# Performance work log

Hardware: AMD Instinct MI355X
Metric: run time of the kernel (lower is better)

The kernel has to match this reference:

```python
import jax, jax.numpy as jnp
import numpy as np

NEG = -1e30  # log-domain 'zero' (safe stand-in for -inf)


def _ctc_loss(logits, labels, label_length, logit_length):
    """Dense-label CTC loss, blank = last class, logits [B,T,C] batch-major.

    Matches tf.nn.ctc_loss(blank_index=-1, logits_time_major=False):
    per-example negative log-likelihood via the standard forward algorithm
    on the blank-extended label sequence of length S = 2L+1.
    """
    B, T, C = logits.shape
    L = labels.shape[1]
    S = 2 * L + 1
    blank = C - 1

    logp = jax.nn.log_softmax(logits, axis=-1)           # [B,T,C]
    lp_t = jnp.moveaxis(logp, 1, 0)                      # [T,B,C]

    # Extended label: blank, l1, blank, l2, ..., blank
    y_ext = jnp.full((B, S), blank, dtype=labels.dtype).at[:, 1::2].set(labels)
    s_idx = jnp.arange(S)
    # s -> s-2 skip allowed iff current symbol is a non-blank differing from s-2
    y_m2 = jnp.pad(y_ext, ((0, 0), (2, 0)), constant_values=blank)[:, :-2]
    skip = (s_idx[None, :] >= 2) & (y_ext != blank) & (y_ext != y_m2)  # [B,S]

    emit0 = jnp.take_along_axis(lp_t[0], y_ext, axis=1)  # [B,S]
    alpha0 = jnp.where(s_idx[None, :] <= 1, emit0, NEG)  # paths start at s=0 or 1

    def step(alpha, lp):
        emit = jnp.take_along_axis(lp, y_ext, axis=1)                      # [B,S]
        a1 = jnp.pad(alpha, ((0, 0), (1, 0)), constant_values=NEG)[:, :-1]  # s-1
        a2 = jnp.pad(alpha, ((0, 0), (2, 0)), constant_values=NEG)[:, :-2]  # s-2
        a2 = jnp.where(skip, a2, NEG)
        new = jnp.logaddexp(jnp.logaddexp(alpha, a1), a2) + emit
        return new, new

    _, alphas = jax.lax.scan(step, alpha0, lp_t[1:])     # [T-1,B,S]
    alphas = jnp.concatenate([alpha0[None], alphas], axis=0)  # [T,B,S]

    b = jnp.arange(B)
    final = alphas[logit_length - 1, b]                  # [B,S] alpha at last frame
    end = 2 * label_length                               # index of final blank
    nll = -jnp.logaddexp(final[b, end], final[b, end - 1])
    return jnp.mean(nll)


def setup_inputs() -> dict:
    key = jax.random.key(0)
    k1, k2, k3 = jax.random.split(key, 3)
    B, T, C, L = 256, 256, 512, 64
    logits = jax.random.normal(k1, (B, T, C), dtype=jnp.float32)
    labels = jax.random.randint(k2, (B, L), 0, C - 1, dtype=jnp.int32)  # never blank
    label_length = jax.random.randint(k3, (B,), 16, L + 1, dtype=jnp.int32)
    logit_length = jnp.full((B,), T, dtype=jnp.int32)
    return {"logits": logits, "labels": labels,
            "label_length": label_length, "logit_length": logit_length}


def reference(logits, labels, label_length, logit_length):
    return _ctc_loss(logits, labels, label_length, logit_length)
```

## Files before the change

kernel.cpp:

```cpp
#include <hip/hip_runtime.h>
#include <math.h>

#define NEGV -1e30f

constexpr int Bc = 256;
constexpr int Tc = 256;
constexpr int Cc = 512;
constexpr int Lc = 64;
constexpr int GR = 8;
constexpr int NGRP = Tc / GR;
constexpr float INVLN2 = 1.44269504088896340736f;
constexpr float LN2    = 0.69314718055994530942f;

__device__ __forceinline__ float la2(float a, float b) {
    float m = fmaxf(a, b);
    float d = fabsf(a - b);
    return m + __log2f(exp2f(-d) + 1.0f);
}

__device__ __forceinline__ float dpp_shr1(float x, float fill) {
    int r = __builtin_amdgcn_update_dpp(__float_as_int(fill), __float_as_int(x),
                                        0x138 , 0xF, 0xF, false);
    return __int_as_float(r);
}

__global__ __launch_bounds__(256) void ctc_k(const float* __restrict__ logits,
                                             const int* __restrict__ labels,
                                             const int* __restrict__ lab_len,
                                             const int* __restrict__ log_len,
                                             float* __restrict__ nll) {
    const int b    = blockIdx.x;
    const int tid  = threadIdx.x;
    const int w    = tid >> 6;
    const int lane = tid & 63;

    __shared__ float rows[2][GR][Cc];
    __shared__ float em_l[2][GR][64];
    __shared__ float em_b[2][GR];

    const float* base = logits + (size_t)b * Tc * Cc;
    const int y = labels[b * Lc + lane];

    const int  prevlab = __shfl_up(y, 1, 64);
    const bool skip    = (lane >= 1) && (y != prevlab);
    const int  llm1    = log_len[b] - 1;
    float ae = NEGV, ao = NEGV, ax = NEGV;
    float fe = NEGV, fo = NEGV, fx = NEGV;

    auto step = [&](float em_lv, float em_bv, int t) {
        float q  = la2(ao, ae);
        float x2 = la2(ax, ao);
        float po = dpp_shr1(ao, NEGV);
        float nae = la2(ae, po) + em_bv;
        float nao = (skip ? la2(q, po) : q) + em_lv;
        float nax = x2 + em_bv;
        ae = nae; ao = nao; ax = nax;
        if (t == llm1) { fe = ae; fo = ao; fx = ax; }
    };

    float4 A0, A1, A2, A3;
    float4 B0, B1, B2, B3;

    auto issue = [&](int g, float4& r0a, float4& r0b, float4& r1a, float4& r1b) {
        const float4* p0 = (const float4*)(base + (size_t)(g * GR + w) * Cc);
        const float4* p1 = (const float4*)(base + (size_t)(g * GR + w + 4) * Cc);
        r0a = p0[lane]; r0b = p0[lane + 64];
        r1a = p1[lane]; r1b = p1[lane + 64];
    };

    auto row_em = [&](int s, int r, const float4& x0, const float4& x1) {
        ((float4*)rows[s][r])[lane]      = x0;
        ((float4*)rows[s][r])[lane + 64] = x1;
        float e = __expf(x0.x) + __expf(x0.y) + __expf(x0.z) + __expf(x0.w)
                + __expf(x1.x) + __expf(x1.y) + __expf(x1.z) + __expf(x1.w);
#pragma unroll
        for (int o = 32; o; o >>= 1) e += __shfl_xor(e, o, 64);
        float lse2 = __log2f(e);
        float xl = rows[s][r][y];
        em_l[s][r][lane] = xl * INVLN2 - lse2;
        if (lane == 63)
            em_b[s][r] = x1.w * INVLN2 - lse2;
    };

    auto finish = [&](int s, const float4& r0a, const float4& r0b,
                             const float4& r1a, const float4& r1b) {
        row_em(s, w,     r0a, r0b);
        row_em(s, w + 4, r1a, r1b);
    };

    auto consume = [&](int i, int s) {
        const int t0 = i * GR;
        if (i == 0) {
            float eb = em_b[0][0];
            float el = em_l[0][0][lane];
            ae = (lane == 0) ? eb : NEGV;
            ao = (lane == 0) ? el : NEGV;
            ax = NEGV;
            if (llm1 == 0) { fe = ae; fo = ao; fx = ax; }
#pragma unroll
            for (int r = 1; r < GR; ++r)
                step(em_l[0][r][lane], em_b[0][r], r);
        } else {
#pragma unroll
            for (int r = 0; r < GR; ++r)
                step(em_l[s][r][lane], em_b[s][r], t0 + r);
        }
    };

    issue(0, A0, A1, A2, A3);
    issue(1, B0, B1, B2, B3);
    finish(0, A0, A1, A2, A3);
    __syncthreads();

    for (int i = 0; i < NGRP; i += 2) {
        if (i + 2 < NGRP) issue(i + 2, A0, A1, A2, A3);
        finish(1, B0, B1, B2, B3);
        if (w == 0) consume(i, 0);
        __syncthreads();

        if (i + 3 < NGRP) issue(i + 3, B0, B1, B2, B3);
        if (i + 2 < NGRP) finish(0, A0, A1, A2, A3);
        if (w == 0) consume(i + 1, 1);
        __syncthreads();
    }

    if (w == 0) {
        const int L  = lab_len[b];
        float f0 = (L == Lc) ? __shfl(fx, 63, 64) : __shfl(fe, L, 64);
        float f1 = __shfl(fo, L - 1, 64);
        if (lane == 0) nll[b] = -LN2 * la2(f0, f1);
    }
}

__global__ __launch_bounds__(256) void reduce_k(const float* __restrict__ nll,
                                                float* __restrict__ out) {
    int tid = threadIdx.x;
    float v = nll[tid];
#pragma unroll
    for (int o = 32; o; o >>= 1) v += __shfl_xor(v, o, 64);
    __shared__ float pr[4];
    if ((tid & 63) == 0) pr[tid >> 6] = v;
    __syncthreads();
    if (tid == 0) out[0] = (pr[0] + pr[1] + pr[2] + pr[3]) * (1.0f / Bc);
}

extern "C" void kernel_launch(void* const* d_in, const int* in_sizes, int n_in,
                              void* d_out, int out_size, void* d_ws, size_t ws_size,
                              hipStream_t stream) {
    const float* logits  = (const float*)d_in[0];
    const int*   labels  = (const int*)d_in[1];
    const int*   lab_len = (const int*)d_in[2];
    const int*   log_len = (const int*)d_in[3];
    float* out = (float*)d_out;
    float* nll = (float*)d_ws;

    hipLaunchKernelGGL(ctc_k, dim3(Bc), dim3(256), 0, stream,
                       logits, labels, lab_len, log_len, nll);
    hipLaunchKernelGGL(reduce_k, dim3(1), dim3(256), 0, stream, nll, out);
}
```

Measured before the change: 222.9 us.

## Split into producer and consumer wavefronts synchronized by shared-memory counters

Turns the block into 8 producer wavefronts, each computing the log-softmax emissions for one time row per step, plus a dedicated consumer wavefront that runs the alpha recursion. They synchronize through per-group atomic counters in shared memory instead of block-wide barriers. The full emission table for all timesteps is kept in LDS (padded to 65 floats per row) so producers can run ahead of the consumer without waiting for it. The intent is to take the serial recursion off the barrier critical path. In exchange the block needs about 80KB of LDS and 576 threads, which cuts occupancy, and the consumer relies on spin-waiting with s_sleep.

```diff
diff --git a/kernel.cpp b/kernel.cpp
--- a/kernel.cpp
+++ b/kernel.cpp
@@ -7,8 +7,9 @@
 constexpr int Tc = 256;
 constexpr int Cc = 512;
 constexpr int Lc = 64;
-constexpr int GR = 8;
-constexpr int NGRP = Tc / GR;
+constexpr int PW = 8;
+constexpr int NGRP = Tc / PW;
+constexpr int EMS = 65;
 constexpr float INVLN2 = 1.44269504088896340736f;
 constexpr float LN2    = 0.69314718055994530942f;
 
@@ -24,7 +25,7 @@
     return __int_as_float(r);
 }
 
-__global__ __launch_bounds__(256) void ctc_k(const float* __restrict__ logits,
+__global__ __launch_bounds__(576) void ctc_k(const float* __restrict__ logits,
                                              const int* __restrict__ labels,
                                              const int* __restrict__ lab_len,
                                              const int* __restrict__ log_len,
@@ -34,97 +35,83 @@
     const int w    = tid >> 6;
     const int lane = tid & 63;
 
-    __shared__ float rows[2][GR][Cc];
-    __shared__ float em_l[2][GR][64];
-    __shared__ float em_b[2][GR];
+    __shared__ float rows[PW][Cc];
+    __shared__ float em[Tc * EMS];
+    __shared__ int   cnt[NGRP];
+
+    if (tid < NGRP) cnt[tid] = 0;
+    __syncthreads();
 
     const float* base = logits + (size_t)b * Tc * Cc;
     const int y = labels[b * Lc + lane];
 
-    const int  prevlab = __shfl_up(y, 1, 64);
-    const bool skip    = (lane >= 1) && (y != prevlab);
-    const int  llm1    = log_len[b] - 1;
-    float ae = NEGV, ao = NEGV, ax = NEGV;
-    float fe = NEGV, fo = NEGV, fx = NEGV;
+    if (w < PW) {
+        float* myrow = rows[w];
+        const float4* p0 = (const float4*)(base + (size_t)w * Cc);
+        float4 c0 = p0[lane], c1 = p0[lane + 64];
+        for (int i = 0; i < NGRP; ++i) {
+            const int t = w + PW * i;
+            float4 n0, n1;
+            if (i + 1 < NGRP) {
+                const float4* pn = (const float4*)(base + (size_t)(t + PW) * Cc);
+                n0 = pn[lane]; n1 = pn[lane + 64];
+            }
+            ((float4*)myrow)[lane]      = c0;
+            ((float4*)myrow)[lane + 64] = c1;
+            float e = __expf(c0.x) + __expf(c0.y) + __expf(c0.z) + __expf(c0.w)
+                    + __expf(c1.x) + __expf(c1.y) + __expf(c1.z) + __expf(c1.w);
+#pragma unroll
+            for (int o = 32; o; o >>= 1) e += __shfl_xor(e, o, 64);
+            float lse2 = __log2f(e);
+            float xl = myrow[y];
+            em[t * EMS + lane] = xl * INVLN2 - lse2;
+            if (lane == 63)
+                em[t * EMS + 64] = c1.w * INVLN2 - lse2;
+            __hip_atomic_fetch_add(&cnt[i], 1, __ATOMIC_RELEASE,
+                                   __HIP_MEMORY_SCOPE_WORKGROUP);
+            c0 = n0; c1 = n1;
+        }
+    } else {
+        const int  prevlab = __shfl_up(y, 1, 64);
+        const bool skip    = (lane >= 1) && (y != prevlab);
+        const int  llm1    = log_len[b] - 1;
+        float ae = NEGV, ao = NEGV, ax = NEGV;
+        float fe = NEGV, fo = NEGV, fx = NEGV;
 
-    auto step = [&](float em_lv, float em_bv, int t) {
-        float q  = la2(ao, ae);
-        float x2 = la2(ax, ao);
-        float po = dpp_shr1(ao, NEGV);
-        float nae = la2(ae, po) + em_bv;
-        float nao = (skip ? la2(q, po) : q) + em_lv;
-        float nax = x2 + em_bv;
-        ae = nae; ao = nao; ax = nax;
-        if (t == llm1) { fe = ae; fo = ao; fx = ax; }
-    };
+        auto step = [&](float em_lv, float em_bv, int t) {
+            float q  = la2(ao, ae);
+            float x2 = la2(ax, ao);
+            float po = dpp_shr1(ao, NEGV);
+            float nae = la2(ae, po) + em_bv;
+            float nao = (skip ? la2(q, po) : q) + em_lv;
+            float nax = x2 + em_bv;
+            ae = nae; ao = nao; ax = nax;
+            if (t == llm1) { fe = ae; fo = ao; fx = ax; }
+        };
 
-    float4 A0, A1, A2, A3;
-    float4 B0, B1, B2, B3;
+        for (int g = 0; g < NGRP; ++g) {
+            while (__hip_atomic_load(&cnt[g], __ATOMIC_ACQUIRE,
+                                     __HIP_MEMORY_SCOPE_WORKGROUP) < PW)
+                __builtin_amdgcn_s_sleep(1);
+            float el[PW], eb[PW];
+#pragma unroll
+            for (int r = 0; r < PW; ++r) {
+                el[r] = em[(PW * g + r) * EMS + lane];
+                eb[r] = em[(PW * g + r) * EMS + 64];
+            }
+            if (g == 0) {
+                ae = (lane == 0) ? eb[0] : NEGV;
+                ao = (lane == 0) ? el[0] : NEGV;
+                ax = NEGV;
+                if (llm1 == 0) { fe = ae; fo = ao; fx = ax; }
+#pragma unroll
+                for (int r = 1; r < PW; ++r) step(el[r], eb[r], r);
+            } else {
+#pragma unroll
+                for (int r = 0; r < PW; ++r) step(el[r], eb[r], PW * g + r);
+            }
+        }
 
-    auto issue = [&](int g, float4& r0a, float4& r0b, float4& r1a, float4& r1b) {
-        const float4* p0 = (const float4*)(base + (size_t)(g * GR + w) * Cc);
-        const float4* p1 = (const float4*)(base + (size_t)(g * GR + w + 4) * Cc);
-        r0a = p0[lane]; r0b = p0[lane + 64];
-        r1a = p1[lane]; r1b = p1[lane + 64];
-    };
-
-    auto row_em = [&](int s, int r, const float4& x0, const float4& x1) {
-        ((float4*)rows[s][r])[lane]      = x0;
-        ((float4*)rows[s][r])[lane + 64] = x1;
-        float e = __expf(x0.x) + __expf(x0.y) + __expf(x0.z) + __expf(x0.w)
-                + __expf(x1.x) + __expf(x1.y) + __expf(x1.z) + __expf(x1.w);
-#pragma unroll
-        for (int o = 32; o; o >>= 1) e += __shfl_xor(e, o, 64);
-        float lse2 = __log2f(e);
-        float xl = rows[s][r][y];
-        em_l[s][r][lane] = xl * INVLN2 - lse2;
-        if (lane == 63)
-            em_b[s][r] = x1.w * INVLN2 - lse2;
-    };
-
-    auto finish = [&](int s, const float4& r0a, const float4& r0b,
-                             const float4& r1a, const float4& r1b) {
-        row_em(s, w,     r0a, r0b);
-        row_em(s, w + 4, r1a, r1b);
-    };
-
-    auto consume = [&](int i, int s) {
-        const int t0 = i * GR;
-        if (i == 0) {
-            float eb = em_b[0][0];
-            float el = em_l[0][0][lane];
-            ae = (lane == 0) ? eb : NEGV;
-            ao = (lane == 0) ? el : NEGV;
-            ax = NEGV;
-            if (llm1 == 0) { fe = ae; fo = ao; fx = ax; }
-#pragma unroll
-            for (int r = 1; r < GR; ++r)
-                step(em_l[0][r][lane], em_b[0][r], r);
-        } else {
-#pragma unroll
-            for (int r = 0; r < GR; ++r)
-                step(em_l[s][r][lane], em_b[s][r], t0 + r);
-        }
-    };
-
-    issue(0, A0, A1, A2, A3);
-    issue(1, B0, B1, B2, B3);
-    finish(0, A0, A1, A2, A3);
-    __syncthreads();
-
-    for (int i = 0; i < NGRP; i += 2) {
-        if (i + 2 < NGRP) issue(i + 2, A0, A1, A2, A3);
-        finish(1, B0, B1, B2, B3);
-        if (w == 0) consume(i, 0);
-        __syncthreads();
-
-        if (i + 3 < NGRP) issue(i + 3, B0, B1, B2, B3);
-        if (i + 2 < NGRP) finish(0, A0, A1, A2, A3);
-        if (w == 0) consume(i + 1, 1);
-        __syncthreads();
-    }
-
-    if (w == 0) {
         const int L  = lab_len[b];
         float f0 = (L == Lc) ? __shfl(fx, 63, 64) : __shfl(fe, L, 64);
         float f1 = __shfl(fo, L - 1, 64);
@@ -154,7 +141,7 @@
     float* out = (float*)d_out;
     float* nll = (float*)d_ws;
 
-    hipLaunchKernelGGL(ctc_k, dim3(Bc), dim3(256), 0, stream,
+    hipLaunchKernelGGL(ctc_k, dim3(Bc), dim3(576), 0, stream,
                        logits, labels, lab_len, log_len, nll);
     hipLaunchKernelGGL(reduce_k, dim3(1), dim3(256), 0, stream, nll, out);
 }
```

After: 198.9 us. 1.12x faster.
